# Performance work log

Measured on AMD Instinct MI355X. Metric: run time of the kernel, lower is better.

The kernel has to match this reference:

```python
import jax, jax.numpy as jnp
import numpy as np

B, Z, A, H = 2048, 64, 8, 512

def setup_inputs() -> dict:
    key = jax.random.key(0)
    ks = jax.random.split(key, 7)
    s = 1.0 / np.sqrt(H).astype(np.float32)
    z = jax.random.normal(ks[0], (B, Z), jnp.float32)
    # PyTorch LSTM params, gate order [i, f, g, o]
    W_ih = jax.random.uniform(ks[1], (4 * H, A + Z), jnp.float32, -s, s)
    W_hh = jax.random.uniform(ks[2], (4 * H, H), jnp.float32, -s, s)
    b_ih = jax.random.uniform(ks[3], (4 * H,), jnp.float32, -s, s)
    b_hh = jax.random.uniform(ks[4], (4 * H,), jnp.float32, -s, s)
    W_out = jax.random.uniform(ks[5], (A, H), jnp.float32, -s, s)
    b_out = jax.random.uniform(ks[6], (A,), jnp.float32, -s, s)
    return {"z": z, "W_ih": W_ih, "W_hh": W_hh, "b_ih": b_ih, "b_hh": b_hh,
            "W_out": W_out, "b_out": b_out, "seq_len": 64}


def reference(z, W_ih, W_hh, b_ih, b_hh, W_out, b_out, seq_len):
    batch = z.shape[0]
    hidden = W_hh.shape[1]
    act = W_out.shape[0]
    # dec_in_t = [zeros_a, z] is identical at every timestep -> hoist input proj
    dec_in = jnp.concatenate([jnp.zeros((batch, act), z.dtype), z], axis=-1)
    x_proj = dec_in @ W_ih.T + b_ih + b_hh  # (B, 4H), constant per step

    def step(carry, _):
        h, c = carry
        gates = x_proj + h @ W_hh.T  # (B, 4H)
        i, f, g, o = jnp.split(gates, 4, axis=-1)
        i = jax.nn.sigmoid(i)
        f = jax.nn.sigmoid(f)
        g = jnp.tanh(g)
        o = jax.nn.sigmoid(o)
        c = f * c + i * g
        h = o * jnp.tanh(c)
        return (h, c), h

    init = (jnp.zeros((batch, hidden), z.dtype), jnp.zeros((batch, hidden), z.dtype))
    _, hs = jax.lax.scan(step, init, None, length=seq_len)  # (T, B, H)
    hs = jnp.transpose(hs, (1, 0, 2))  # (B, T, H)
    return hs @ W_out.T + b_out  # (B, T, A)
```

## Files before the change

kernel.cpp:

```cpp
#include <hip/hip_runtime.h>


#define HID   512
#define TSTEP 64
#define KCAT  576

typedef unsigned long long u64;
typedef __attribute__((ext_vector_type(8))) short bf16x8;
typedef __attribute__((ext_vector_type(4))) float f32x4;

__device__ inline unsigned short f2bf(float f) {
  unsigned int u = __builtin_bit_cast(unsigned int, f);
  unsigned int r = (u + 0x7fffu + ((u >> 16) & 1u)) >> 16;
  return (unsigned short)r;
}
__device__ inline float sigm(float x) { return 1.0f / (1.0f + __expf(-x)); }
__device__ inline float tanh_f(float x) { return 1.0f - 2.0f / (__expf(2.0f * x) + 1.0f); }

__device__ inline void gl16(const unsigned short* g, unsigned short* l) {
  __builtin_amdgcn_global_load_lds(
      (const __attribute__((address_space(1))) unsigned int*)g,
      (__attribute__((address_space(3))) unsigned int*)l, 16, 0, 0);
}
__device__ inline void ldc16(bf16x8& d, const unsigned short* p) {
  asm volatile("global_load_dwordx4 %0, %1, off sc0 sc1"
               : "=v"(d) : "v"(p) : "memory");
}

#define ATOMLD(PTR) __hip_atomic_load((PTR), __ATOMIC_RELAXED, __HIP_MEMORY_SCOPE_AGENT)
#define ATOMST(PTR, V) __hip_atomic_store((PTR), (V), __ATOMIC_RELAXED, __HIP_MEMORY_SCOPE_AGENT)
#define WAITV(N) do { asm volatile("s_waitcnt vmcnt(" #N ")" ::: "memory"); \
                      __builtin_amdgcn_sched_barrier(0); } while (0)

__global__ void k_prep(const float* __restrict__ z, const float* __restrict__ wih,
                       const float* __restrict__ whh, const float* __restrict__ bih,
                       const float* __restrict__ bhh,
                       unsigned short* __restrict__ wcat, unsigned short* __restrict__ zbf,
                       float* __restrict__ bias) {
  int c = blockIdx.x * 256 + threadIdx.x;
  if (c < 147456) {
    int n = c / 72, kc = (c % 72) * 8;
    unsigned short u[8];
#pragma unroll
    for (int e = 0; e < 8; ++e) {
      int k = kc + e;
      float v = (k < 512) ? whh[(size_t)n * 512 + k] : wih[(size_t)n * 72 + 8 + (k - 512)];
      u[e] = f2bf(v);
    }
    *(bf16x8*)&wcat[(size_t)n * KCAT + kc] = *(bf16x8*)u;
  } else if (c < 163840) {
    int i = c - 147456;
    int row = i >> 3, kc = (i & 7) * 8;
    unsigned short u[8];
#pragma unroll
    for (int e = 0; e < 8; ++e) u[e] = f2bf(z[(size_t)row * 64 + kc + e]);
    *(bf16x8*)&zbf[(size_t)row * 64 + kc] = *(bf16x8*)u;
  } else if (c < 165888) {
    int n = c - 163840;
    bias[n] = bih[n] + bhh[n];
  }
}

__global__ void k_zero(int* __restrict__ flags) {
  int g = blockIdx.x * 256 + threadIdx.x;
  if (g < TSTEP * 512) flags[g] = 0;
}

struct P {
  const unsigned short *wcat, *zbf;
  const float *bias, *wout, *bout;
  unsigned short *h0, *h1;
  float* out;
  int* flags;
};

#define SMEM_SZ 70656

__global__ __launch_bounds__(256, 2) void k_persist(P p) {
  extern __shared__ char smem[];
  unsigned short* Bb[3] = {(unsigned short*)smem, (unsigned short*)(smem + 16384),
                           (unsigned short*)(smem + 32768)};
  unsigned short* wo = (unsigned short*)(smem + 49152);
  unsigned short* hO = (unsigned short*)(smem + 65536);

  const int bid = blockIdx.x;
  const int nt = bid >> 5, bt = bid & 31;
  const int tid = threadIdx.x;
  const int lane = tid & 63;
  const int wv = tid >> 6;
  const int mq = wv >> 1, nh = wv & 1;
  const int cl = lane & 15, q8 = lane >> 4;
  const int b0 = bt * 64, j0 = nt * 32;
  const int c0 = nt >> 1;

  const int rS = tid >> 3;
  const int xS = ((tid & 7) ^ (rS & 7)) * 8;
  const unsigned short* srcB[4];
#pragma unroll
  for (int k = 0; k < 4; ++k) {
    int rB = k * 32 + rS;
    int n = (rB >> 5) * HID + j0 + (rB & 31);
    srcB[k] = p.wcat + (size_t)n * KCAT + xS;
  }
#define STAGEB(BUF, CHUNK) { _Pragma("unroll") for (int k4 = 0; k4 < 4; ++k4) \
    gl16(srcB[k4] + (CHUNK) * 64, &Bb[BUF][(k4 * 256 + wv * 64) * 8]); }

  if (nt == 0) {
    int r = tid >> 4, s0 = tid & 15;
#pragma unroll
    for (int i = 0; i < 4; ++i) {
      int s = s0 + i * 16;
      unsigned short u[8] = {0, 0, 0, 0, 0, 0, 0, 0};
      if (r < 8) {
        const float* wp = p.wout + (size_t)r * 512 + s * 8;
        float4 f0 = *(const float4*)wp;
        float4 f1 = *(const float4*)(wp + 4);
        u[0] = f2bf(f0.x); u[1] = f2bf(f0.y); u[2] = f2bf(f0.z); u[3] = f2bf(f0.w);
        u[4] = f2bf(f1.x); u[5] = f2bf(f1.y); u[6] = f2bf(f1.z); u[7] = f2bf(f1.w);
      }
      int off = r * 512 + (s >> 3) * 64 + (((s & 7) ^ (r & 7)) * 8);
      *(bf16x8*)&wo[off] = *(bf16x8*)u;
    }
  }
  bf16x8 azr[4];
#pragma unroll
  for (int m = 0; m < 2; ++m)
#pragma unroll
    for (int ks = 0; ks < 2; ++ks)
      azr[m * 2 + ks] = *(const bf16x8*)&p.zbf[(size_t)(b0 + mq * 32 + m * 16 + cl) * 64 + ks * 32 + q8 * 8];

  float bias_r[4];
#pragma unroll
  for (int g = 0; g < 4; ++g) bias_r[g] = p.bias[g * HID + j0 + nh * 16 + cl];
  f32x4 c0v = {0, 0, 0, 0}, c1v = {0, 0, 0, 0};
  f32x4 acc[4][2];
  f32x4 accp0, accp1;
  const float boutv = (cl < 8) ? p.bout[cl] : 0.0f;
  const int arow = tid >> 2, aseg = tid & 3;
  const int r0 = b0 + mq * 32 + cl;

  bf16x8 ra[3][4];
  auto issueA = [&](bf16x8 d[4], const unsigned short* hp, int kk) {
    const unsigned short* base0 = hp + (size_t)r0 * HID + kk * 64 + q8 * 8;
    const unsigned short* base1 = base0 + 16 * HID;
    ldc16(d[0], base0);
    ldc16(d[1], base0 + 32);
    ldc16(d[2], base1);
    ldc16(d[3], base1 + 32);
  };

  auto gate_mfma = [&](const bf16x8 a4[4], const unsigned short* Bl, int kkv) {
    __builtin_amdgcn_s_setprio(1);
#pragma unroll
    for (int ks = 0; ks < 2; ++ks) {
      const int sx = ((ks * 4 + q8) ^ (cl & 7)) * 8;
      bf16x8 af0 = a4[ks], af1 = a4[2 + ks];
#pragma unroll
      for (int g = 0; g < 4; ++g) {
        bf16x8 bf = *(const bf16x8*)&Bl[(g * 32 + nh * 16 + cl) * 64 + sx];
        acc[g][0] = __builtin_amdgcn_mfma_f32_16x16x32_bf16(af0, bf, acc[g][0], 0, 0, 0);
        acc[g][1] = __builtin_amdgcn_mfma_f32_16x16x32_bf16(af1, bf, acc[g][1], 0, 0, 0);
      }
      if (nt == 0 && nh == 0 && kkv < 8) {
        bf16x8 wf = *(const bf16x8*)&wo[cl * 512 + kkv * 64 + sx];
        accp0 = __builtin_amdgcn_mfma_f32_16x16x32_bf16(af0, wf, accp0, 0, 0, 0);
        accp1 = __builtin_amdgcn_mfma_f32_16x16x32_bf16(af1, wf, accp1, 0, 0, 0);
      }
    }
    __builtin_amdgcn_s_setprio(0);
  };

  auto cell_store_flag = [&](unsigned short* hcur, int t) {
#pragma unroll
    for (int fm = 0; fm < 2; ++fm) {
      f32x4 cold = fm ? c1v : c0v;
      f32x4 cn;
#pragma unroll
      for (int r = 0; r < 4; ++r) {
        float iv = sigm(acc[0][fm][r]);
        float fv = sigm(acc[1][fm][r]);
        float gv = tanh_f(acc[2][fm][r]);
        float ov = sigm(acc[3][fm][r]);
        float cv = fv * cold[r] + iv * gv;
        cn[r] = cv;
        hO[(mq * 32 + fm * 16 + q8 * 4 + r) * 40 + nh * 16 + cl] = f2bf(ov * tanh_f(cv));
      }
      if (fm) c1v = cn; else c0v = cn;
    }
    __syncthreads();
    u64 u0 = *(const u64*)&hO[arow * 40 + aseg * 8];
    u64 u1 = *(const u64*)&hO[arow * 40 + aseg * 8 + 4];
    u64* dst = (u64*)(hcur + (size_t)(b0 + arow) * HID + j0 + aseg * 8);
    ATOMST(dst, u0);
    ATOMST(dst + 1, u1);
    STAGEB(0, c0);
    STAGEB(1, (c0 + 1) & 7);
    WAITV(8);
    __builtin_amdgcn_s_barrier();
    if (tid == 0)
      ATOMST(&p.flags[t * 512 + bt * 16 + nt], 1);
  };

  STAGEB(2, 8);
  asm volatile("s_waitcnt vmcnt(0) lgkmcnt(0)" ::: "memory");
  __builtin_amdgcn_sched_barrier(0);
  __builtin_amdgcn_s_barrier();
#pragma unroll
  for (int g = 0; g < 4; ++g) {
    f32x4 v = {bias_r[g], bias_r[g], bias_r[g], bias_r[g]};
    acc[g][0] = v; acc[g][1] = v;
  }
  gate_mfma(azr, Bb[2], 8);
  cell_store_flag(p.h0, 0);

  for (int t = 1; t < TSTEP; ++t) {
    const unsigned short* hprev = (t & 1) ? p.h0 : p.h1;
    unsigned short* hcur = (t & 1) ? p.h1 : p.h0;
    const int* fbase = &p.flags[(t - 1) * 512 + bt * 16];

    if (tid < 8) {
      int rcq = (c0 + (tid >> 1)) & 7;
      const int* fp = fbase + rcq * 2 + (tid & 1);
      while (ATOMLD(fp) == 0) __builtin_amdgcn_s_sleep(1);
    }
    __syncthreads();

    issueA(ra[0], hprev, c0);
    issueA(ra[1], hprev, (c0 + 1) & 7);
    issueA(ra[2], hprev, (c0 + 2) & 7);
    WAITV(8);
    __builtin_amdgcn_s_barrier();

#pragma unroll
    for (int g = 0; g < 4; ++g) {
      f32x4 v = {bias_r[g], bias_r[g], bias_r[g], bias_r[g]};
      acc[g][0] = v; acc[g][1] = v;
    }
    { f32x4 v = {boutv, boutv, boutv, boutv}; accp0 = v; accp1 = v; }

#pragma unroll
    for (int j = 0; j <= 8; ++j) {
      const int rcj = (c0 + j) & 7;
      gate_mfma(j < 8 ? ra[j % 3] : azr, Bb[j % 3], j < 8 ? rcj : 8);
      if (j == 8) break;
      if (j <= 4) issueA(ra[j % 3], hprev, (c0 + j + 3) & 7);
      if (j <= 6) STAGEB((j + 2) % 3, (j + 2 < 8) ? ((c0 + j + 2) & 7) : 8);
      if (j <= 3 && tid < 2) {
        const int* fp = fbase + ((c0 + j + 4) & 7) * 2 + tid;
        while (ATOMLD(fp) == 0) __builtin_amdgcn_s_sleep(1);
      }
      if (j == 0)      WAITV(12);
      else if (j <= 4) WAITV(8);
      else if (j <= 6) WAITV(4);
      else             WAITV(0);
      __builtin_amdgcn_s_barrier();
    }

    if (nt == 0 && nh == 0 && cl < 8) {
      const int tt = t - 1;
#pragma unroll
      for (int r = 0; r < 4; ++r) {
        int b = b0 + mq * 32 + q8 * 4 + r;
        p.out[((size_t)b * 64 + tt) * 8 + cl] = accp0[r];
        p.out[((size_t)(b + 16) * 64 + tt) * 8 + cl] = accp1[r];
      }
    }
    cell_store_flag(hcur, t);
  }

  if (nt == 0) {
    if (tid < 16) {
      const int* fp = &p.flags[63 * 512 + bt * 16 + tid];
      while (ATOMLD(fp) == 0) __builtin_amdgcn_s_sleep(1);
    }
    __syncthreads();
    const unsigned short* h63 = p.h1;
    issueA(ra[0], h63, 0);
    issueA(ra[1], h63, 1);
    issueA(ra[2], h63, 2);
    f32x4 ap0 = {boutv, boutv, boutv, boutv};
    f32x4 ap1 = ap0;
#pragma unroll
    for (int kk = 0; kk < 8; ++kk) {
      if (kk <= 5)      WAITV(8);
      else if (kk == 6) WAITV(4);
      else              WAITV(0);
      if (nh == 0) {
#pragma unroll
        for (int ks = 0; ks < 2; ++ks) {
          const int sx = ((ks * 4 + q8) ^ (cl & 7)) * 8;
          bf16x8 wf = *(const bf16x8*)&wo[cl * 512 + kk * 64 + sx];
          ap0 = __builtin_amdgcn_mfma_f32_16x16x32_bf16(ra[kk % 3][ks], wf, ap0, 0, 0, 0);
          ap1 = __builtin_amdgcn_mfma_f32_16x16x32_bf16(ra[kk % 3][2 + ks], wf, ap1, 0, 0, 0);
        }
      }
      if (kk <= 4) issueA(ra[kk % 3], h63, kk + 3);
    }
    if (nh == 0 && cl < 8) {
#pragma unroll
      for (int r = 0; r < 4; ++r) {
        int b = b0 + mq * 32 + q8 * 4 + r;
        p.out[((size_t)b * 64 + 63) * 8 + cl] = ap0[r];
        p.out[((size_t)(b + 16) * 64 + 63) * 8 + cl] = ap1[r];
      }
    }
  }
#undef STAGEB
}

template <int GATES, int PROJ>
__global__ __launch_bounds__(256, 2) void k_stepF(
    const unsigned short* __restrict__ hprev, unsigned short* __restrict__ hnext,
    const unsigned short* __restrict__ wcat, const unsigned short* __restrict__ zbf,
    const float* __restrict__ wout, const float* __restrict__ bias,
    const float* __restrict__ bout, float* __restrict__ cst,
    float* __restrict__ out, int t) {
  __shared__ unsigned short Ab[2][64 * 64];
  __shared__ unsigned short Bb[2][128 * 64];
  __shared__ unsigned short wo_lds[16 * 512];
  __shared__ unsigned short hO[64 * 40];

  const int bid = blockIdx.x;
  const int nt = GATES ? (((bid & 7) << 1) | ((bid >> 8) & 1)) : 0;
  const int bt = GATES ? ((bid >> 3) & 31) : bid;
  const int tid = threadIdx.x;
  const int lane = tid & 63;
  const int wv = tid >> 6;
  const int mq = wv >> 1, nh = wv & 1;
  const int cl = lane & 15, q8 = lane >> 4;
  const int b0 = bt * 64, j0 = nt * 32;

  const int rA = tid >> 3;
  const int xA = ((tid & 7) ^ (rA & 7)) * 8;
  const unsigned short* srcA0 = hprev + (size_t)(b0 + rA) * HID + xA;
  const unsigned short* srcA1 = hprev + (size_t)(b0 + 32 + rA) * HID + xA;
  const unsigned short* srcZ0 = zbf + (size_t)(b0 + rA) * 64 + xA;
  const unsigned short* srcZ1 = zbf + (size_t)(b0 + 32 + rA) * 64 + xA;
  const unsigned short* srcB[4];
#pragma unroll
  for (int k = 0; k < 4; ++k) {
    int rB = k * 32 + rA;
    int n = (rB >> 5) * HID + j0 + (rB & 31);
    srcB[k] = wcat + (size_t)n * KCAT + xA;
  }

  auto do_stage = [&](int buf, int kkv) {
    if (GATES) {
      if (kkv == 8) {
        gl16(srcZ0, &Ab[buf][(wv * 64) * 8]);
        gl16(srcZ1, &Ab[buf][(256 + wv * 64) * 8]);
      } else {
        gl16(srcA0 + kkv * 64, &Ab[buf][(wv * 64) * 8]);
        gl16(srcA1 + kkv * 64, &Ab[buf][(256 + wv * 64) * 8]);
      }
#pragma unroll
      for (int k = 0; k < 4; ++k)
        gl16(srcB[k] + kkv * 64, &Bb[buf][(k * 256 + wv * 64) * 8]);
    } else {
      gl16(srcA0 + kkv * 64, &Ab[buf][(wv * 64) * 8]);
      gl16(srcA1 + kkv * 64, &Ab[buf][(256 + wv * 64) * 8]);
    }
  };

  if (PROJ) {
    int r = tid >> 4, s0 = tid & 15;
#pragma unroll
    for (int i = 0; i < 4; ++i) {
      int s = s0 + i * 16;
      unsigned short u[8] = {0, 0, 0, 0, 0, 0, 0, 0};
      if (r < 8) {
        const float* wp = wout + (size_t)r * 512 + s * 8;
        float4 f0 = *(const float4*)wp;
        float4 f1 = *(const float4*)(wp + 4);
        u[0] = f2bf(f0.x); u[1] = f2bf(f0.y); u[2] = f2bf(f0.z); u[3] = f2bf(f0.w);
        u[4] = f2bf(f1.x); u[5] = f2bf(f1.y); u[6] = f2bf(f1.z); u[7] = f2bf(f1.w);
      }
      int off = r * 512 + (s >> 3) * 64 + (((s & 7) ^ (r & 7)) * 8);
      *(bf16x8*)&wo_lds[off] = *(bf16x8*)u;
    }
  }

  f32x4 acc[4][2];
  if (GATES) {
#pragma unroll
    for (int g = 0; g < 4; ++g) {
      float bv = bias[g * HID + j0 + nh * 16 + cl];
      f32x4 v = {bv, bv, bv, bv};
      acc[g][0] = v; acc[g][1] = v;
    }
  }
  f32x4 accp0 = {0, 0, 0, 0}, accp1 = {0, 0, 0, 0};
  if (PROJ) {
    float bo = (cl < 8) ? bout[cl] : 0.0f;
    f32x4 v = {bo, bo, bo, bo};
    accp0 = v; accp1 = v;
  }

  const size_t cbase = ((size_t)bid * 256 + tid) * 8;
  f32x4 c0 = {0, 0, 0, 0}, c1 = {0, 0, 0, 0};
  if (GATES && t > 0) { c0 = *(const f32x4*)&cst[cbase]; c1 = *(const f32x4*)&cst[cbase + 4]; }

  auto mfma_block = [&](int bu, int kkv) {
    const unsigned short* Al = Ab[bu];
    const unsigned short* Bl = Bb[bu];
#pragma unroll
    for (int ks = 0; ks < 2; ++ks) {
      const int sx = ((ks * 4 + q8) ^ (cl & 7)) * 8;
      bf16x8 af0 = *(const bf16x8*)&Al[(mq * 32 + cl) * 64 + sx];
      bf16x8 af1 = *(const bf16x8*)&Al[(mq * 32 + 16 + cl) * 64 + sx];
      if (GATES) {
#pragma unroll
        for (int g = 0; g < 4; ++g) {
          bf16x8 bf = *(const bf16x8*)&Bl[(g * 32 + nh * 16 + cl) * 64 + sx];
          acc[g][0] = __builtin_amdgcn_mfma_f32_16x16x32_bf16(af0, bf, acc[g][0], 0, 0, 0);
          acc[g][1] = __builtin_amdgcn_mfma_f32_16x16x32_bf16(af1, bf, acc[g][1], 0, 0, 0);
        }
      }
      if (PROJ && nh == 0 && kkv < 8) {
        bf16x8 wf = *(const bf16x8*)&wo_lds[cl * 512 + kkv * 64 + sx];
        accp0 = __builtin_amdgcn_mfma_f32_16x16x32_bf16(af0, wf, accp0, 0, 0, 0);
        accp1 = __builtin_amdgcn_mfma_f32_16x16x32_bf16(af1, wf, accp1, 0, 0, 0);
      }
    }
  };

  if (GATES && t == 0) {
    do_stage(0, 8);
    asm volatile("s_waitcnt vmcnt(0) lgkmcnt(0)" ::: "memory");
    __builtin_amdgcn_s_barrier();
    mfma_block(0, 8);
  } else {
    do_stage(0, 0);
    do_stage(1, 1);
    if (GATES) asm volatile("s_waitcnt vmcnt(6) lgkmcnt(0)" ::: "memory");
    else       asm volatile("s_waitcnt vmcnt(2) lgkmcnt(0)" ::: "memory");
    __builtin_amdgcn_s_barrier();
    const int kkEnd = GATES ? 8 : 7;
    for (int kk = 0;; ++kk) {
      mfma_block(kk & 1, kk);
      if (kk == kkEnd) break;
      asm volatile("" ::: "memory");
      __builtin_amdgcn_s_barrier();
      if (kk + 2 <= kkEnd) {
        do_stage(kk & 1, kk + 2);
        if (GATES) asm volatile("s_waitcnt vmcnt(6)" ::: "memory");
        else       asm volatile("s_waitcnt vmcnt(2)" ::: "memory");
      } else {
        asm volatile("s_waitcnt vmcnt(0)" ::: "memory");
      }
      asm volatile("" ::: "memory");
      __builtin_amdgcn_s_barrier();
    }
  }

  if (PROJ && nh == 0 && cl < 8) {
    const int tt = t - 1;
#pragma unroll
    for (int r = 0; r < 4; ++r) {
      int b = b0 + mq * 32 + q8 * 4 + r;
      out[((size_t)b * 64 + tt) * 8 + cl] = accp0[r];
      out[((size_t)(b + 16) * 64 + tt) * 8 + cl] = accp1[r];
    }
  }

  if (GATES) {
#pragma unroll
    for (int fm = 0; fm < 2; ++fm) {
      f32x4 cold = fm ? c1 : c0;
      f32x4 cn;
#pragma unroll
      for (int r = 0; r < 4; ++r) {
        float iv = sigm(acc[0][fm][r]);
        float fv = sigm(acc[1][fm][r]);
        float gv = tanh_f(acc[2][fm][r]);
        float ov = sigm(acc[3][fm][r]);
        float cv = fv * cold[r] + iv * gv;
        cn[r] = cv;
        hO[(mq * 32 + fm * 16 + q8 * 4 + r) * 40 + nh * 16 + cl] = f2bf(ov * tanh_f(cv));
      }
      if (fm) c1 = cn; else c0 = cn;
    }
    *(f32x4*)&cst[cbase] = c0;
    *(f32x4*)&cst[cbase + 4] = c1;
    __syncthreads();
    int row = tid >> 2, sg4 = tid & 3;
    unsigned short tmp[8];
#pragma unroll
    for (int e = 0; e < 8; ++e) tmp[e] = hO[row * 40 + sg4 * 8 + e];
    *(int4*)&hnext[(size_t)(b0 + row) * HID + j0 + sg4 * 8] = *(int4*)tmp;
  }
}

extern "C" void kernel_launch(void* const* d_in, const int* in_sizes, int n_in,
                              void* d_out, int out_size, void* d_ws, size_t ws_size,
                              hipStream_t stream) {
  const float* z    = (const float*)d_in[0];
  const float* wih  = (const float*)d_in[1];
  const float* whh  = (const float*)d_in[2];
  const float* bih  = (const float*)d_in[3];
  const float* bhh  = (const float*)d_in[4];
  const float* wout = (const float*)d_in[5];
  const float* bout = (const float*)d_in[6];
  float* out = (float*)d_out;

  char* ws = (char*)d_ws;
  unsigned short* wcat = (unsigned short*)(ws);
  unsigned short* zbf  = (unsigned short*)(ws + 2359296);
  float* bias          = (float*)(ws + 2621440);
  unsigned short* h0   = (unsigned short*)(ws + 2629632);
  unsigned short* h1   = (unsigned short*)(ws + 4726784);
  int* flags           = (int*)(ws + 6823936);
  float* cst           = (float*)(ws + 6955008);

  k_prep<<<dim3(648), dim3(256), 0, stream>>>(z, wih, whh, bih, bhh, wcat, zbf, bias);
  k_zero<<<dim3(128), dim3(256), 0, stream>>>(flags);

  P pp;
  pp.wcat = wcat; pp.zbf = zbf; pp.bias = bias; pp.wout = wout; pp.bout = bout;
  pp.h0 = h0; pp.h1 = h1; pp.out = out; pp.flags = flags;

  hipFuncSetAttribute((const void*)k_persist,
                      hipFuncAttributeMaxDynamicSharedMemorySize, SMEM_SZ);
  void* args[] = {&pp};
  hipError_t e = hipLaunchCooperativeKernel((const void*)k_persist, dim3(512), dim3(256),
                                            args, SMEM_SZ, stream);
  if (e == hipSuccess) return;

  for (int t = 0; t < TSTEP; ++t) {
    const unsigned short* hp = (t & 1) ? h0 : h1;
    unsigned short* hn = (t & 1) ? h1 : h0;
    if (t == 0)
      k_stepF<1, 0><<<dim3(512), dim3(256), 0, stream>>>(hp, hn, wcat, zbf, wout, bias,
                                                         bout, cst, out, t);
    else
      k_stepF<1, 1><<<dim3(512), dim3(256), 0, stream>>>(hp, hn, wcat, zbf, wout, bias,
                                                         bout, cst, out, t);
  }
  k_stepF<0, 1><<<dim3(32), dim3(256), 0, stream>>>(h1, h0, wcat, zbf, wout, bias,
                                                    bout, cst, out, TSTEP);
}
```

Measured before the change: 901.2 us.

## Keep full weight slice resident in LDS with 512-thread persistent blocks

The persistent kernel goes from 512 blocks of 256 threads to 256 blocks of 512 threads, each handling 128 batch rows. Each block now loads its entire 9-chunk weight slice (144KB) into LDS once, so the per-timestep global-to-LDS weight streaming and its barriers go away. W_out fragments are held in registers, and the flag array and synchronization are resized to match. The risks are the large LDS footprint and launch_bounds(512,2), which may not fit two blocks per CU or may cause register spills, and fewer blocks taking part in each step.

Result: faster. 784.7 us (-12.9%).

```diff
diff --git a/kernel.cpp b/kernel.cpp
--- a/kernel.cpp
+++ b/kernel.cpp
@@ -63,7 +63,7 @@
 
 __global__ void k_zero(int* __restrict__ flags) {
   int g = blockIdx.x * 256 + threadIdx.x;
-  if (g < TSTEP * 512) flags[g] = 0;
+  if (g < TSTEP * 256) flags[g] = 0;
 }
 
 struct P {
@@ -74,61 +74,61 @@
   int* flags;
 };
 
-#define SMEM_SZ 70656
-
-__global__ __launch_bounds__(256, 2) void k_persist(P p) {
+#define SMEM_SZ 157696
+
+__global__ __launch_bounds__(512, 2) void k_persist(P p) {
   extern __shared__ char smem[];
-  unsigned short* Bb[3] = {(unsigned short*)smem, (unsigned short*)(smem + 16384),
-                           (unsigned short*)(smem + 32768)};
-  unsigned short* wo = (unsigned short*)(smem + 49152);
-  unsigned short* hO = (unsigned short*)(smem + 65536);
+#define WPL(KK) ((unsigned short*)(smem + (KK) * 16384))
+  unsigned short* hO = (unsigned short*)(smem + 147456);
 
   const int bid = blockIdx.x;
-  const int nt = bid >> 5, bt = bid & 31;
+  const int nt = bid >> 4, bt = bid & 15;
   const int tid = threadIdx.x;
   const int lane = tid & 63;
   const int wv = tid >> 6;
   const int mq = wv >> 1, nh = wv & 1;
   const int cl = lane & 15, q8 = lane >> 4;
-  const int b0 = bt * 64, j0 = nt * 32;
-  const int c0 = nt >> 1;
-
-  const int rS = tid >> 3;
-  const int xS = ((tid & 7) ^ (rS & 7)) * 8;
-  const unsigned short* srcB[4];
-#pragma unroll
-  for (int k = 0; k < 4; ++k) {
-    int rB = k * 32 + rS;
-    int n = (rB >> 5) * HID + j0 + (rB & 31);
-    srcB[k] = p.wcat + (size_t)n * KCAT + xS;
-  }
-#define STAGEB(BUF, CHUNK) { _Pragma("unroll") for (int k4 = 0; k4 < 4; ++k4) \
-    gl16(srcB[k4] + (CHUNK) * 64, &Bb[BUF][(k4 * 256 + wv * 64) * 8]); }
-
-  if (nt == 0) {
-    int r = tid >> 4, s0 = tid & 15;
-#pragma unroll
-    for (int i = 0; i < 4; ++i) {
-      int s = s0 + i * 16;
-      unsigned short u[8] = {0, 0, 0, 0, 0, 0, 0, 0};
-      if (r < 8) {
-        const float* wp = p.wout + (size_t)r * 512 + s * 8;
-        float4 f0 = *(const float4*)wp;
-        float4 f1 = *(const float4*)(wp + 4);
-        u[0] = f2bf(f0.x); u[1] = f2bf(f0.y); u[2] = f2bf(f0.z); u[3] = f2bf(f0.w);
-        u[4] = f2bf(f1.x); u[5] = f2bf(f1.y); u[6] = f2bf(f1.z); u[7] = f2bf(f1.w);
-      }
-      int off = r * 512 + (s >> 3) * 64 + (((s & 7) ^ (r & 7)) * 8);
-      *(bf16x8*)&wo[off] = *(bf16x8*)u;
-    }
-  }
+  const int b0 = bt * 128, j0 = nt * 32;
+  const int c0 = (nt == 0) ? 0 : (nt >> 1);
+
+  {
+    const int rS = tid >> 3;
+    const int xS = ((tid & 7) ^ (rS & 7)) * 8;
+    int n0 = (rS >> 5) * HID + j0 + (rS & 31);
+    int n1 = ((rS + 64) >> 5) * HID + j0 + ((rS + 64) & 31);
+    const unsigned short* s0 = p.wcat + (size_t)n0 * KCAT + xS;
+    const unsigned short* s1 = p.wcat + (size_t)n1 * KCAT + xS;
+#pragma unroll
+    for (int kk = 0; kk < 9; ++kk) {
+      gl16(s0 + kk * 64, &WPL(kk)[(wv * 64) * 8]);
+      gl16(s1 + kk * 64, &WPL(kk)[(512 + wv * 64) * 8]);
+    }
+  }
+
+  bf16x8 wfr[8][2];
+  if (nt == 0 && nh == 0) {
+#pragma unroll
+    for (int kk = 0; kk < 8; ++kk)
+#pragma unroll
+      for (int ks = 0; ks < 2; ++ks) {
+        unsigned short u[8] = {0, 0, 0, 0, 0, 0, 0, 0};
+        if (cl < 8) {
+          const float* wp = p.wout + (size_t)cl * 512 + kk * 64 + ks * 32 + q8 * 8;
+          float4 f0 = *(const float4*)wp;
+          float4 f1 = *(const float4*)(wp + 4);
+          u[0] = f2bf(f0.x); u[1] = f2bf(f0.y); u[2] = f2bf(f0.z); u[3] = f2bf(f0.w);
+          u[4] = f2bf(f1.x); u[5] = f2bf(f1.y); u[6] = f2bf(f1.z); u[7] = f2bf(f1.w);
+        }
+        wfr[kk][ks] = *(bf16x8*)u;
+      }
+  }
+
   bf16x8 azr[4];
 #pragma unroll
   for (int m = 0; m < 2; ++m)
 #pragma unroll
     for (int ks = 0; ks < 2; ++ks)
       azr[m * 2 + ks] = *(const bf16x8*)&p.zbf[(size_t)(b0 + mq * 32 + m * 16 + cl) * 64 + ks * 32 + q8 * 8];
-
   float bias_r[4];
 #pragma unroll
   for (int g = 0; g < 4; ++g) bias_r[g] = p.bias[g * HID + j0 + nh * 16 + cl];
@@ -139,7 +139,7 @@
   const int arow = tid >> 2, aseg = tid & 3;
   const int r0 = b0 + mq * 32 + cl;
 
-  bf16x8 ra[3][4];
+  bf16x8 ra[4][4];
   auto issueA = [&](bf16x8 d[4], const unsigned short* hp, int kk) {
     const unsigned short* base0 = hp + (size_t)r0 * HID + kk * 64 + q8 * 8;
     const unsigned short* base1 = base0 + 16 * HID;
@@ -149,7 +149,7 @@
     ldc16(d[3], base1 + 32);
   };
 
-  auto gate_mfma = [&](const bf16x8 a4[4], const unsigned short* Bl, int kkv) {
+  auto gate_mfma = [&](const bf16x8 a4[4], const unsigned short* Bl, int jph, bool isz) {
     __builtin_amdgcn_s_setprio(1);
 #pragma unroll
     for (int ks = 0; ks < 2; ++ks) {
@@ -161,10 +161,9 @@
         acc[g][0] = __builtin_amdgcn_mfma_f32_16x16x32_bf16(af0, bf, acc[g][0], 0, 0, 0);
         acc[g][1] = __builtin_amdgcn_mfma_f32_16x16x32_bf16(af1, bf, acc[g][1], 0, 0, 0);
       }
-      if (nt == 0 && nh == 0 && kkv < 8) {
-        bf16x8 wf = *(const bf16x8*)&wo[cl * 512 + kkv * 64 + sx];
-        accp0 = __builtin_amdgcn_mfma_f32_16x16x32_bf16(af0, wf, accp0, 0, 0, 0);
-        accp1 = __builtin_amdgcn_mfma_f32_16x16x32_bf16(af1, wf, accp1, 0, 0, 0);
+      if (nt == 0 && nh == 0 && !isz) {
+        accp0 = __builtin_amdgcn_mfma_f32_16x16x32_bf16(af0, wfr[jph][ks], accp0, 0, 0, 0);
+        accp1 = __builtin_amdgcn_mfma_f32_16x16x32_bf16(af1, wfr[jph][ks], accp1, 0, 0, 0);
       }
     }
     __builtin_amdgcn_s_setprio(0);
@@ -193,15 +192,12 @@
     u64* dst = (u64*)(hcur + (size_t)(b0 + arow) * HID + j0 + aseg * 8);
     ATOMST(dst, u0);
     ATOMST(dst + 1, u1);
-    STAGEB(0, c0);
-    STAGEB(1, (c0 + 1) & 7);
-    WAITV(8);
+    WAITV(0);
     __builtin_amdgcn_s_barrier();
     if (tid == 0)
-      ATOMST(&p.flags[t * 512 + bt * 16 + nt], 1);
+      ATOMST(&p.flags[t * 256 + bt * 16 + nt], 1);
   };
 
-  STAGEB(2, 8);
   asm volatile("s_waitcnt vmcnt(0) lgkmcnt(0)" ::: "memory");
   __builtin_amdgcn_sched_barrier(0);
   __builtin_amdgcn_s_barrier();
@@ -210,17 +206,14 @@
     f32x4 v = {bias_r[g], bias_r[g], bias_r[g], bias_r[g]};
     acc[g][0] = v; acc[g][1] = v;
   }
-  gate_mfma(azr, Bb[2], 8);
+  gate_mfma(azr, WPL(8), 0, true);
   cell_store_flag(p.h0, 0);
 
   for (int t = 1; t < TSTEP; ++t) {
     const unsigned short* hprev = (t & 1) ? p.h0 : p.h1;
     unsigned short* hcur = (t & 1) ? p.h1 : p.h0;
-    const int* fbase = &p.flags[(t - 1) * 512 + bt * 16];
-
-    if (tid < 8) {
-      int rcq = (c0 + (tid >> 1)) & 7;
-      const int* fp = fbase + rcq * 2 + (tid & 1);
+    if (tid < 16) {
+      const int* fp = &p.flags[(t - 1) * 256 + bt * 16 + tid];
       while (ATOMLD(fp) == 0) __builtin_amdgcn_s_sleep(1);
     }
     __syncthreads();
@@ -228,8 +221,7 @@
     issueA(ra[0], hprev, c0);
     issueA(ra[1], hprev, (c0 + 1) & 7);
     issueA(ra[2], hprev, (c0 + 2) & 7);
-    WAITV(8);
-    __builtin_amdgcn_s_barrier();
+    issueA(ra[3], hprev, (c0 + 3) & 7);
 
 #pragma unroll
     for (int g = 0; g < 4; ++g) {
@@ -240,20 +232,13 @@
 
 #pragma unroll
     for (int j = 0; j <= 8; ++j) {
-      const int rcj = (c0 + j) & 7;
-      gate_mfma(j < 8 ? ra[j % 3] : azr, Bb[j % 3], j < 8 ? rcj : 8);
-      if (j == 8) break;
-      if (j <= 4) issueA(ra[j % 3], hprev, (c0 + j + 3) & 7);
-      if (j <= 6) STAGEB((j + 2) % 3, (j + 2 < 8) ? ((c0 + j + 2) & 7) : 8);
-      if (j <= 3 && tid < 2) {
-        const int* fp = fbase + ((c0 + j + 4) & 7) * 2 + tid;
-        while (ATOMLD(fp) == 0) __builtin_amdgcn_s_sleep(1);
-      }
-      if (j == 0)      WAITV(12);
-      else if (j <= 4) WAITV(8);
-      else if (j <= 6) WAITV(4);
-      else             WAITV(0);
-      __builtin_amdgcn_s_barrier();
+      if (j <= 4)      WAITV(12);
+      else if (j == 5) WAITV(8);
+      else if (j == 6) WAITV(4);
+      else if (j == 7) WAITV(0);
+      const unsigned short* Bl = (j < 8) ? WPL((c0 + j) & 7) : WPL(8);
+      gate_mfma(j < 8 ? ra[j & 3] : azr, Bl, j < 8 ? j : 0, j == 8);
+      if (j <= 3) issueA(ra[j & 3], hprev, (c0 + j + 4) & 7);
     }
 
     if (nt == 0 && nh == 0 && cl < 8) {
@@ -270,42 +255,42 @@
 
   if (nt == 0) {
     if (tid < 16) {
-      const int* fp = &p.flags[63 * 512 + bt * 16 + tid];
+      const int* fp = &p.flags[63 * 256 + bt * 16 + tid];
       while (ATOMLD(fp) == 0) __builtin_amdgcn_s_sleep(1);
     }
     __syncthreads();
     const unsigned short* h63 = p.h1;
-    issueA(ra[0], h63, 0);
-    issueA(ra[1], h63, 1);
-    issueA(ra[2], h63, 2);
     f32x4 ap0 = {boutv, boutv, boutv, boutv};
     f32x4 ap1 = ap0;
-#pragma unroll
-    for (int kk = 0; kk < 8; ++kk) {
-      if (kk <= 5)      WAITV(8);
-      else if (kk == 6) WAITV(4);
-      else              WAITV(0);
-      if (nh == 0) {
+    if (nh == 0) {
+      issueA(ra[0], h63, 0);
+      issueA(ra[1], h63, 1);
+      issueA(ra[2], h63, 2);
+      issueA(ra[3], h63, 3);
+#pragma unroll
+      for (int kk = 0; kk < 8; ++kk) {
+        if (kk <= 4)      WAITV(12);
+        else if (kk == 5) WAITV(8);
+        else if (kk == 6) WAITV(4);
+        else              WAITV(0);
 #pragma unroll
         for (int ks = 0; ks < 2; ++ks) {
-          const int sx = ((ks * 4 + q8) ^ (cl & 7)) * 8;
-          bf16x8 wf = *(const bf16x8*)&wo[cl * 512 + kk * 64 + sx];
-          ap0 = __builtin_amdgcn_mfma_f32_16x16x32_bf16(ra[kk % 3][ks], wf, ap0, 0, 0, 0);
-          ap1 = __builtin_amdgcn_mfma_f32_16x16x32_bf16(ra[kk % 3][2 + ks], wf, ap1, 0, 0, 0);
+          ap0 = __builtin_amdgcn_mfma_f32_16x16x32_bf16(ra[kk & 3][ks], wfr[kk][ks], ap0, 0, 0, 0);
+          ap1 = __builtin_amdgcn_mfma_f32_16x16x32_bf16(ra[kk & 3][2 + ks], wfr[kk][ks], ap1, 0, 0, 0);
         }
-      }
-      if (kk <= 4) issueA(ra[kk % 3], h63, kk + 3);
-    }
-    if (nh == 0 && cl < 8) {
-#pragma unroll
-      for (int r = 0; r < 4; ++r) {
-        int b = b0 + mq * 32 + q8 * 4 + r;
-        p.out[((size_t)b * 64 + 63) * 8 + cl] = ap0[r];
-        p.out[((size_t)(b + 16) * 64 + 63) * 8 + cl] = ap1[r];
-      }
-    }
-  }
-#undef STAGEB
+        if (kk <= 3) issueA(ra[kk & 3], h63, kk + 4);
+      }
+      if (cl < 8) {
+#pragma unroll
+        for (int r = 0; r < 4; ++r) {
+          int b = b0 + mq * 32 + q8 * 4 + r;
+          p.out[((size_t)b * 64 + 63) * 8 + cl] = ap0[r];
+          p.out[((size_t)(b + 16) * 64 + 63) * 8 + cl] = ap1[r];
+        }
+      }
+    }
+  }
+#undef WPL
 }
 
 template <int GATES, int PROJ>
@@ -510,10 +495,10 @@
   unsigned short* h0   = (unsigned short*)(ws + 2629632);
   unsigned short* h1   = (unsigned short*)(ws + 4726784);
   int* flags           = (int*)(ws + 6823936);
-  float* cst           = (float*)(ws + 6955008);
+  float* cst           = (float*)(ws + 6889472);
 
   k_prep<<<dim3(648), dim3(256), 0, stream>>>(z, wih, whh, bih, bhh, wcat, zbf, bias);
-  k_zero<<<dim3(128), dim3(256), 0, stream>>>(flags);
+  k_zero<<<dim3(64), dim3(256), 0, stream>>>(flags);
 
   P pp;
   pp.wcat = wcat; pp.zbf = zbf; pp.bias = bias; pp.wout = wout; pp.bout = bout;
@@ -522,7 +507,7 @@
   hipFuncSetAttribute((const void*)k_persist,
                       hipFuncAttributeMaxDynamicSharedMemorySize, SMEM_SZ);
   void* args[] = {&pp};
-  hipError_t e = hipLaunchCooperativeKernel((const void*)k_persist, dim3(512), dim3(256),
+  hipError_t e = hipLaunchCooperativeKernel((const void*)k_persist, dim3(256), dim3(512),
                                             args, SMEM_SZ, stream);
   if (e == hipSuccess) return;
 
```
